# Optimization experiments

Hardware: AMD Instinct MI355X
Metric: run time of the kernel (lower is better)

The kernel has to match this reference:

```python
import jax, jax.numpy as jnp
import numpy as np

B, C, H, W = 8, 64, 224, 224
M, N = 7, 7          # kernel_size
S = 2                # stride
NEG_INF = -1e30      # aggregation identity for max-plus (finite, fp-safe); unused since pad=0


def setup_inputs() -> dict:
    key = jax.random.key(0)
    kx, kw = jax.random.split(key)
    x = jax.random.normal(kx, (B, C, H, W), dtype=jnp.float32)
    w = jax.random.normal(kw, (1, C, M, N), dtype=jnp.float32)  # (B_w=1, C_out, M, N)
    return {"x": x, "w": w}


def reference(x, w):
    """SemiPool2d with max-plus semifield, padding='valid', ceil_mode=False.

    out[b,c,p,q] = max_{i<M, j<N} ( x[b,c, p*S+i, q*S+j] + w[0,c,i,j] )
    """
    Bf, Cin, Hx, Wx = x.shape
    _, Cout, Mk, Nk = w.shape
    H_out = (Hx - Mk) // S + 1
    W_out = (Wx - Nk) // S + 1
    # pad_h = max((H_out-1)*S + M - H, 0) = 0 for these dims -> no padding needed.
    # Unfold: gather the MN strided shifts (small fixed loop over kernel taps).
    patches = jnp.stack(
        [x[:, :, i:i + S * (H_out - 1) + 1:S, j:j + S * (W_out - 1) + 1:S]
         for i in range(Mk) for j in range(Nk)],
        axis=2,
    )  # (B, C, M*N, H_out, W_out)
    # weighting = '+', aggregation = max over the window taps (dim 3 in original)
    weighted = patches + w.reshape(1, Cout, Mk * Nk, 1, 1)
    return jnp.max(weighted, axis=2)  # (B, C_out, H_out, W_out)
```

## Files before the change

### kernel.cpp

```cpp
#include <hip/hip_runtime.h>


#define HH 224
#define WW 224
#define HO 109
#define WO 109
#define CC 64
#define PBAND 16
#define NB 7
#define INROWS (2*PBAND + 5)
#define LDSF (INROWS*WW)
#define CHUNKS (LDSF/4)
#define ITERS (CHUNKS/256)
#define TAIL (CHUNKS - ITERS*256)

__global__ __launch_bounds__(256) void semipool_kernel(
    const float* __restrict__ x,
    const float* __restrict__ w,
    float* __restrict__ out)
{
    __shared__ float smem[LDSF];

    const int tid  = threadIdx.x;
    const int band = blockIdx.x >> 9;
    const int bc   = blockIdx.x & 511;

    int p0b = band * PBAND;
    if (p0b > HO - PBAND) p0b = HO - PBAND;
    const int row0 = 2 * p0b;

    const float* src = x + (bc * HH + row0) * WW;
#pragma unroll
    for (int it = 0; it < ITERS; ++it) {
        int c = it * 256 + tid;
        __builtin_amdgcn_global_load_lds(
            (const __attribute__((address_space(1))) void*)(src + 4 * c),
            (__attribute__((address_space(3))) void*)(smem + 4 * c),
            16, 0, 0);
    }
    if (tid < TAIL) {
        int c = ITERS * 256 + tid;
        __builtin_amdgcn_global_load_lds(
            (const __attribute__((address_space(1))) void*)(src + 4 * c),
            (__attribute__((address_space(3))) void*)(smem + 4 * c),
            16, 0, 0);
    }

    const float* __restrict__ wp = w + (bc & (CC - 1)) * 49;
    float wr[49];
#pragma unroll
    for (int k = 0; k < 49; ++k) wr[k] = wp[k];

    __syncthreads();

    int q = tid & 127; if (q > WO - 1) q = WO - 1;
    const int ph   = tid >> 7;
    const int p0t  = p0b + 8 * ph;
    const int colb = 2 * q;

    float acc[8];
#pragma unroll
    for (int a = 0; a < 8; ++a) acc[a] = -1e30f;

#pragma unroll
    for (int r = 0; r < 21; ++r) {
        const float* lr = smem + (16 * ph + r) * WW + colb;
        float xr[8];
#pragma unroll
        for (int k = 0; k < 4; ++k) {
            float2 v = *reinterpret_cast<const float2*>(lr + 2 * k);
            xr[2 * k]     = v.x;
            xr[2 * k + 1] = v.y;
        }
#pragma unroll
        for (int pp = 0; pp < 8; ++pp) {
            int i = r - 2 * pp;
            if (i >= 0 && i < 7) {
                float s0 = xr[0] + wr[i * 7 + 0];
                float s1 = xr[1] + wr[i * 7 + 1];
                float s2 = xr[2] + wr[i * 7 + 2];
                float s3 = xr[3] + wr[i * 7 + 3];
                float s4 = xr[4] + wr[i * 7 + 4];
                float s5 = xr[5] + wr[i * 7 + 5];
                float s6 = xr[6] + wr[i * 7 + 6];
                float t0 = fmaxf(fmaxf(s0, s1), s2);
                float t1 = fmaxf(fmaxf(s3, s4), s5);
                float t2 = fmaxf(fmaxf(t0, t1), s6);
                acc[pp] = fmaxf(acc[pp], t2);
            }
        }
    }

    float* __restrict__ orow = out + (bc * HO + p0t) * WO + q;
#pragma unroll
    for (int pp = 0; pp < 8; ++pp)
        orow[pp * WO] = acc[pp];
}

extern "C" void kernel_launch(void* const* d_in, const int* in_sizes, int n_in,
                              void* d_out, int out_size, void* d_ws, size_t ws_size,
                              hipStream_t stream) {
    const float* x = (const float*)d_in[0];
    const float* w = (const float*)d_in[1];
    float* out = (float*)d_out;

    int blocks = NB * 512;
    semipool_kernel<<<blocks, 256, 0, stream>>>(x, w, out);
}
```

Measured before the change: 27.12 us.

## Double-buffer LDS row bands with persistent per-channel blocks

Replaces the one-shot load of a 16-output-row band per block with a loop over 7 bands of 8 output rows each. Each block now handles half the rows of one (batch, channel) plane. Two LDS buffers are filled with async global-to-LDS loads, so the next band is fetched while the current one is computed, with explicit vmcnt waits and barriers between stages. The grid shrinks to 1024 blocks, and the weights are loaded once per block. The cost is extra halo traffic: smaller bands re-read more overlapping input rows. There is also less block-level parallelism and two barriers per band.

```diff
diff --git a/kernel.cpp b/kernel.cpp
--- a/kernel.cpp
+++ b/kernel.cpp
@@ -6,95 +6,119 @@
 #define HO 109
 #define WO 109
 #define CC 64
-#define PBAND 16
-#define NB 7
-#define INROWS (2*PBAND + 5)
-#define LDSF (INROWS*WW)
-#define CHUNKS (LDSF/4)
-#define ITERS (CHUNKS/256)
-#define TAIL (CHUNKS - ITERS*256)
+#define PBAND 8
+#define NT 7
+#define INROWS 21
+#define BANDF (INROWS*WW)
+#define WCHUNK 294
+#define STAGE_INSTR 5
 
 __global__ __launch_bounds__(256) void semipool_kernel(
     const float* __restrict__ x,
     const float* __restrict__ w,
     float* __restrict__ out)
 {
-    __shared__ float smem[LDSF];
+    __shared__ float smem[2][BANDF];
 
     const int tid  = threadIdx.x;
-    const int band = blockIdx.x >> 9;
-    const int bc   = blockIdx.x & 511;
+    const int wv   = tid >> 6;
+    const int lane = tid & 63;
+    const int half = blockIdx.x & 1;
+    const int bc   = blockIdx.x >> 1;
 
-    int p0b = band * PBAND;
-    if (p0b > HO - PBAND) p0b = HO - PBAND;
-    const int row0 = 2 * p0b;
-
-    const float* src = x + (bc * HH + row0) * WW;
-#pragma unroll
-    for (int it = 0; it < ITERS; ++it) {
-        int c = it * 256 + tid;
-        __builtin_amdgcn_global_load_lds(
-            (const __attribute__((address_space(1))) void*)(src + 4 * c),
-            (__attribute__((address_space(3))) void*)(smem + 4 * c),
-            16, 0, 0);
-    }
-    if (tid < TAIL) {
-        int c = ITERS * 256 + tid;
-        __builtin_amdgcn_global_load_lds(
-            (const __attribute__((address_space(1))) void*)(src + 4 * c),
-            (__attribute__((address_space(3))) void*)(smem + 4 * c),
-            16, 0, 0);
-    }
+    const float* __restrict__ xc = x + bc * (HH * WW);
 
     const float* __restrict__ wp = w + (bc & (CC - 1)) * 49;
     float wr[49];
 #pragma unroll
     for (int k = 0; k < 49; ++k) wr[k] = wp[k];
 
-    __syncthreads();
-
     int q = tid & 127; if (q > WO - 1) q = WO - 1;
     const int ph   = tid >> 7;
-    const int p0t  = p0b + 8 * ph;
     const int colb = 2 * q;
 
-    float acc[8];
+#define STAGE(BUF, P0)                                                        \
+    do {                                                                      \
+        const float* _src = xc + (2 * (P0)) * WW;                             \
+        _Pragma("unroll")                                                     \
+        for (int it = 0; it < STAGE_INSTR; ++it) {                            \
+            int off = it * 64 + lane;                                         \
+            if (off < WCHUNK) {                                               \
+                int c = wv * WCHUNK + off;                                    \
+                __builtin_amdgcn_global_load_lds(                             \
+                    (const __attribute__((address_space(1))) void*)(_src + 4 * c), \
+                    (__attribute__((address_space(3))) void*)(&smem[BUF][4 * c]),  \
+                    16, 0, 0);                                                \
+            }                                                                 \
+        }                                                                     \
+    } while (0)
+
+    const int band0 = half * NT;
+    {
+        int p00 = band0 * PBAND; if (p00 > HO - PBAND) p00 = HO - PBAND;
+        STAGE(0, p00);
+    }
+
+#pragma unroll 1
+    for (int t = 0; t < NT; ++t) {
+        const int cur = t & 1;
+        int p0 = (band0 + t) * PBAND; if (p0 > HO - PBAND) p0 = HO - PBAND;
+
+        if (t + 1 < NT) {
+            int p0n = (band0 + t + 1) * PBAND;
+            if (p0n > HO - PBAND) p0n = HO - PBAND;
+            STAGE(cur ^ 1, p0n);
+            asm volatile("s_waitcnt vmcnt(5)" ::: "memory");
+        } else {
+            asm volatile("s_waitcnt vmcnt(0)" ::: "memory");
+        }
+        __builtin_amdgcn_sched_barrier(0);
+        __builtin_amdgcn_s_barrier();
+        __builtin_amdgcn_sched_barrier(0);
+
+        const float* __restrict__ sb = &smem[cur][0] + (8 * ph) * WW + colb;
+        float acc[4];
 #pragma unroll
-    for (int a = 0; a < 8; ++a) acc[a] = -1e30f;
+        for (int a = 0; a < 4; ++a) acc[a] = -1e30f;
 
 #pragma unroll
-    for (int r = 0; r < 21; ++r) {
-        const float* lr = smem + (16 * ph + r) * WW + colb;
-        float xr[8];
+        for (int rr = 0; rr < 13; ++rr) {
+            const float* lr = sb + rr * WW;
+            float xr[8];
 #pragma unroll
-        for (int k = 0; k < 4; ++k) {
-            float2 v = *reinterpret_cast<const float2*>(lr + 2 * k);
-            xr[2 * k]     = v.x;
-            xr[2 * k + 1] = v.y;
-        }
+            for (int k = 0; k < 4; ++k) {
+                float2 v = *reinterpret_cast<const float2*>(lr + 2 * k);
+                xr[2 * k]     = v.x;
+                xr[2 * k + 1] = v.y;
+            }
 #pragma unroll
-        for (int pp = 0; pp < 8; ++pp) {
-            int i = r - 2 * pp;
-            if (i >= 0 && i < 7) {
-                float s0 = xr[0] + wr[i * 7 + 0];
-                float s1 = xr[1] + wr[i * 7 + 1];
-                float s2 = xr[2] + wr[i * 7 + 2];
-                float s3 = xr[3] + wr[i * 7 + 3];
-                float s4 = xr[4] + wr[i * 7 + 4];
-                float s5 = xr[5] + wr[i * 7 + 5];
-                float s6 = xr[6] + wr[i * 7 + 6];
-                float t0 = fmaxf(fmaxf(s0, s1), s2);
-                float t1 = fmaxf(fmaxf(s3, s4), s5);
-                float t2 = fmaxf(fmaxf(t0, t1), s6);
-                acc[pp] = fmaxf(acc[pp], t2);
+            for (int pp = 0; pp < 4; ++pp) {
+                int i = rr - 2 * pp;
+                if (i >= 0 && i < 7) {
+                    float s0 = xr[0] + wr[i * 7 + 0];
+                    float s1 = xr[1] + wr[i * 7 + 1];
+                    float s2 = xr[2] + wr[i * 7 + 2];
+                    float s3 = xr[3] + wr[i * 7 + 3];
+                    float s4 = xr[4] + wr[i * 7 + 4];
+                    float s5 = xr[5] + wr[i * 7 + 5];
+                    float s6 = xr[6] + wr[i * 7 + 6];
+                    float t0 = fmaxf(fmaxf(s0, s1), s2);
+                    float t1 = fmaxf(fmaxf(s3, s4), s5);
+                    float t2 = fmaxf(fmaxf(t0, t1), s6);
+                    acc[pp] = fmaxf(acc[pp], t2);
+                }
             }
         }
+
+        float* __restrict__ orow = out + (bc * HO + p0 + 4 * ph) * WO + q;
+#pragma unroll
+        for (int pp = 0; pp < 4; ++pp)
+            orow[pp * WO] = acc[pp];
+
+        __builtin_amdgcn_sched_barrier(0);
+        __builtin_amdgcn_s_barrier();
+        __builtin_amdgcn_sched_barrier(0);
     }
-
-    float* __restrict__ orow = out + (bc * HO + p0t) * WO + q;
-#pragma unroll
-    for (int pp = 0; pp < 8; ++pp)
-        orow[pp * WO] = acc[pp];
 }
 
 extern "C" void kernel_launch(void* const* d_in, const int* in_sizes, int n_in,
@@ -104,6 +128,5 @@
     const float* w = (const float*)d_in[1];
     float* out = (float*)d_out;
 
-    int blocks = NB * 512;
-    semipool_kernel<<<blocks, 256, 0, stream>>>(x, w, out);
+    semipool_kernel<<<1024, 256, 0, stream>>>(x, w, out);
 }
```

Result: slower. 28.59 us (+5.4%).
